# Performance work log

Hardware: AMD Instinct MI355X
Metric: run time of the kernel (lower is better)

The kernel has to match this reference:

```python
import jax, jax.numpy as jnp
import numpy as np

NG = 65160
NM = 10242   # mesh nodes (icosphere splits=5)
N = NG + NM
F = 156      # num_timesteps * num_features = 2 * 78
FI = 3       # init (lat/lon) feature size
H = 128
OUT = 78
B = 2
E_ENC, E_PROC, E_DEC = 130320, 81920, 195480


def gcn_conv(X, src, dst, W, b, num_nodes):
    """PyG GCNConv: add self-loops, symmetric D^-1/2 (A+I) D^-1/2 normalization.
    X: [B, N, Fin]; src/dst: [E] int; W: [Fin, Fout]; b: [Fout]."""
    loop = jnp.arange(num_nodes, dtype=src.dtype)
    s = jnp.concatenate([src, loop])
    d = jnp.concatenate([dst, loop])
    deg = jax.ops.segment_sum(jnp.ones(d.shape, X.dtype), d, num_segments=num_nodes)
    dinv = jax.lax.rsqrt(deg)  # deg >= 1 thanks to self-loops
    norm = dinv[s] * dinv[d]   # [E+N]
    XW = X @ W                 # [B, N, Fout]
    msg = XW[:, s, :] * norm[None, :, None]          # gather + scale
    agg = jax.vmap(lambda m: jax.ops.segment_sum(m, d, num_segments=num_nodes))(msg)
    return agg + b


def mlp2(X, w1, b1, w2, b2):
    return jax.nn.relu(X @ w1 + b1) @ w2 + b2


def setup_inputs() -> dict:
    key = jax.random.key(0)
    ks = jax.random.split(key, 32)
    def w(k, i, o):
        return jax.random.normal(k, (i, o), jnp.float32) / np.float32(np.sqrt(i))
    def bvec(k, o):
        return jax.random.normal(k, (o,), jnp.float32) * 0.01
    inp = {
        'X': jax.random.normal(ks[0], (B, NG, F), jnp.float32),
        'init_grid_features': jax.random.normal(ks[1], (NG, FI), jnp.float32),
        'init_mesh_features': jax.random.normal(ks[2], (NM, FI), jnp.float32),
        'enc_mlp_w1': w(ks[3], F + FI, H), 'enc_mlp_b1': bvec(ks[4], H),
        'enc_mlp_w2': w(ks[5], H, H),      'enc_mlp_b2': bvec(ks[6], H),
        'enc_gcn_w1': w(ks[7], H, H),      'enc_gcn_b1': bvec(ks[8], H),
        'enc_gcn_w2': w(ks[9], H, H),      'enc_gcn_b2': bvec(ks[10], H),
        'proc_gcn_w1': w(ks[11], H, H),    'proc_gcn_b1': bvec(ks[12], H),
        'proc_gcn_w2': w(ks[13], H, H),    'proc_gcn_b2': bvec(ks[14], H),
        'dec_gcn_w1': w(ks[15], H, H),     'dec_gcn_b1': bvec(ks[16], H),
        'dec_gcn_w2': w(ks[17], H, OUT),   'dec_gcn_b2': bvec(ks[18], OUT),
        # encoding graph: bipartite grid -> mesh (mesh indices offset by NG)
        'enc_src': jax.random.randint(ks[19], (E_ENC,), 0, NG, jnp.int32),
        'enc_dst': NG + jax.random.randint(ks[20], (E_ENC,), 0, NM, jnp.int32),
        # processing graph: mesh -> mesh (local indices over mesh nodes)
        'proc_src': jax.random.randint(ks[21], (E_PROC,), 0, NM, jnp.int32),
        'proc_dst': jax.random.randint(ks[22], (E_PROC,), 0, NM, jnp.int32),
        # decoding graph: bipartite mesh -> grid
        'dec_src': NG + jax.random.randint(ks[23], (E_DEC,), 0, NM, jnp.int32),
        'dec_dst': jax.random.randint(ks[24], (E_DEC,), 0, NG, jnp.int32),
    }
    return inp


def reference(X, init_grid_features, init_mesh_features,
              enc_mlp_w1, enc_mlp_b1, enc_mlp_w2, enc_mlp_b2,
              enc_gcn_w1, enc_gcn_b1, enc_gcn_w2, enc_gcn_b2,
              proc_gcn_w1, proc_gcn_b1, proc_gcn_w2, proc_gcn_b2,
              dec_gcn_w1, dec_gcn_b1, dec_gcn_w2, dec_gcn_b2,
              enc_src, enc_dst, proc_src, proc_dst, dec_src, dec_dst):
    b = X.shape[0]
    # _preprocess_input: grid feats + init grid feats ; zero mesh feats + init mesh feats
    grid = jnp.concatenate(
        [X, jnp.broadcast_to(init_grid_features[None], (b, NG, FI))], axis=-1)
    mesh = jnp.concatenate(
        [jnp.zeros((b, NM, F), X.dtype),
         jnp.broadcast_to(init_mesh_features[None], (b, NM, FI))], axis=-1)
    Xall = jnp.concatenate([grid, mesh], axis=1)  # [B, N, F+FI]
    # encoder: MLP then 2-layer GCN on full (grid+mesh) node set
    h = mlp2(Xall, enc_mlp_w1, enc_mlp_b1, enc_mlp_w2, enc_mlp_b2)
    h = jax.nn.relu(gcn_conv(h, enc_src, enc_dst, enc_gcn_w1, enc_gcn_b1, N))
    h = gcn_conv(h, enc_src, enc_dst, enc_gcn_w2, enc_gcn_b2, N)
    grid_h, mesh_h = h[:, :NG, :], h[:, NG:, :]
    # processor: 2-layer GCN on mesh nodes only
    m = jax.nn.relu(gcn_conv(mesh_h, proc_src, proc_dst, proc_gcn_w1, proc_gcn_b1, NM))
    m = gcn_conv(m, proc_src, proc_dst, proc_gcn_w2, proc_gcn_b2, NM)
    # decoder: 2-layer GCN on concatenated (grid, processed mesh) nodes
    pf = jnp.concatenate([grid_h, m], axis=1)  # [B, N, H]
    d1 = jax.nn.relu(gcn_conv(pf, dec_src, dec_dst, dec_gcn_w1, dec_gcn_b1, N))
    out = gcn_conv(d1, dec_src, dec_dst, dec_gcn_w2, dec_gcn_b2, N)
    return out[:, :NG, :]  # [B, NG, OUT]
```

## Files before the change

### kernel.cpp

```cpp
#include <hip/hip_runtime.h>
#include <hip/hip_bf16.h>

#define NGRID  65160
#define NMESH  10242
#define NTOT   75402
#define FEAT   156
#define FI_    3
#define KENC   159
#define HD     128
#define OUTD   78
#define BB     2
#define NE_ENC 130320
#define NE_PROC 81920
#define NE_DEC 195480

typedef __attribute__((ext_vector_type(8))) short bf16x8;
typedef __attribute__((ext_vector_type(4))) float f32x4;

__device__ __forceinline__ short bf16_rtn(float v) {
    unsigned u = __builtin_bit_cast(unsigned, v);
    u += 0x7FFFu + ((u >> 16) & 1u);
    return (short)(u >> 16);
}
__device__ __forceinline__ float bf16_f32(short s) {
    unsigned u = ((unsigned)(unsigned short)s) << 16;
    return __builtin_bit_cast(float, u);
}

__global__ void wprep_kernel(const float* __restrict__ W, int K, int Nc,
                             short* __restrict__ WTh, short* __restrict__ WTl,
                             int KP, int NP)
{
    int idx = blockIdx.x * 256 + threadIdx.x;
    if (idx >= KP * NP) return;
    int c = idx / KP;
    int k = idx - c * KP;
    float v = (k < K && c < Nc) ? W[k * Nc + c] : 0.0f;
    short h = bf16_rtn(v);
    WTh[idx] = h;
    WTl[idx] = bf16_rtn(v - bf16_f32(h));
}

__global__ void zero_kernel(int* __restrict__ p, int n) {
    int i = blockIdx.x * 256 + threadIdx.x;
    if (i < n) p[i] = 0;
}

__global__ void count_kernel(const int* __restrict__ dst, int* __restrict__ cnt, int ne) {
    int e = blockIdx.x * 256 + threadIdx.x;
    if (e < ne) atomicAdd(&cnt[dst[e]], 1);
}

__global__ __launch_bounds__(256)
void scan1_kernel(const int* __restrict__ in, int* __restrict__ out,
                  int* __restrict__ bsum, int n)
{
    __shared__ int ws[256];
    const int t = threadIdx.x;
    const int base = blockIdx.x * 1024 + t * 4;
    int v[4], s = 0;
#pragma unroll
    for (int j = 0; j < 4; ++j) {
        int i = base + j;
        v[j] = (i < n) ? in[i] : 0;
        s += v[j];
    }
    ws[t] = s;
    __syncthreads();
    for (int off = 1; off < 256; off <<= 1) {
        int x = (t >= off) ? ws[t - off] : 0;
        __syncthreads();
        ws[t] += x;
        __syncthreads();
    }
    int excl = ws[t] - s;
#pragma unroll
    for (int j = 0; j < 4; ++j) {
        int i = base + j;
        if (i < n) out[i] = excl;
        excl += v[j];
    }
    if (t == 255) bsum[blockIdx.x] = ws[255];
}

__global__ __launch_bounds__(256)
void scan2_kernel(int* __restrict__ bsum, int nb)
{
    __shared__ int ws[256];
    const int t = threadIdx.x;
    int s = (t < nb) ? bsum[t] : 0;
    ws[t] = s;
    __syncthreads();
    for (int off = 1; off < 256; off <<= 1) {
        int x = (t >= off) ? ws[t - off] : 0;
        __syncthreads();
        ws[t] += x;
        __syncthreads();
    }
    if (t < nb) bsum[t] = ws[t] - s;
}

__global__ __launch_bounds__(256)
void scan3_kernel(int* __restrict__ out, const int* __restrict__ bsum, int n)
{
    int i = blockIdx.x * 256 + threadIdx.x;
    if (i < n) out[i] += bsum[i >> 10];
}

__global__ void dinv_kernel(const int* __restrict__ cnt, float* __restrict__ dinv, int n) {
    int i = blockIdx.x * 256 + threadIdx.x;
    if (i < n) dinv[i] = rsqrtf(1.0f + (float)cnt[i]);
}

__global__ void fillcsr_kernel(const int* __restrict__ src, const int* __restrict__ dst,
                               const int* __restrict__ rowptr, int* __restrict__ fill,
                               int* __restrict__ colsrc, int ne) {
    int e = blockIdx.x * 256 + threadIdx.x;
    if (e < ne) {
        int d = dst[e];
        int pos = atomicAdd(&fill[d], 1);
        colsrc[rowptr[d] + pos] = src[e];
    }
}

template<int KP, int NOUT, int MODE, int RELU_OUT>
__global__ __launch_bounds__(256)
void gemm_mfma(const float* __restrict__ A0, long long a0_bs,
               const float* __restrict__ A1, long long a1_bs, int split,
               const float* __restrict__ Xin, const float* __restrict__ GFin,
               const float* __restrict__ MFin,
               const short* __restrict__ WTh, const short* __restrict__ WTl,
               const float* __restrict__ bias,
               float* __restrict__ Qout, long long q_bs,
               int rows_per_batch, int total_rows)
{
    constexpr int NCT = (NOUT + 15) / 16;
    const int t = threadIdx.x;
    const int w = t >> 6;
    const int l = t & 63;
    const int lane15 = l & 15;
    const int g = l >> 4;

    const int gr_a = blockIdx.x * 64 + w * 16 + lane15;
    const bool a_valid = (gr_a < total_rows);
    int b_a = 0, r_a = 0;
    const float* arow = nullptr;
    if (a_valid) {
        b_a = gr_a / rows_per_batch;
        r_a = gr_a - b_a * rows_per_batch;
        if (MODE == 0) {
            arow = A0 + b_a * a0_bs + (long long)r_a * KP;
        } else if (MODE == 2) {
            if (r_a >= split) arow = A1 + b_a * a1_bs + (long long)(r_a - split) * KP;
            else              arow = A0 + b_a * a0_bs + (long long)r_a * KP;
        }
    }

    f32x4 acc[NCT];
#pragma unroll
    for (int ct = 0; ct < NCT; ++ct) acc[ct] = (f32x4){0.f, 0.f, 0.f, 0.f};

#pragma unroll
    for (int k0 = 0; k0 < KP; k0 += 32) {
        const int kbase = k0 + g * 8;
        float av[8];
        if (MODE == 1) {
#pragma unroll
            for (int j = 0; j < 8; ++j) av[j] = 0.0f;
            if (a_valid) {
                const bool gridr = (r_a < NGRID);
                if (gridr && kbase + 8 <= FEAT) {
                    const float* xrow = Xin + ((long long)b_a * NGRID + r_a) * FEAT + kbase;
#pragma unroll
                    for (int j2 = 0; j2 < 4; ++j2) {
                        float2 v = *(const float2*)(xrow + j2 * 2);
                        av[j2 * 2]     = v.x;
                        av[j2 * 2 + 1] = v.y;
                    }
                } else {
#pragma unroll
                    for (int j = 0; j < 8; ++j) {
                        int k = kbase + j;
                        float v = 0.0f;
                        if (k < FEAT) {
                            if (gridr) v = Xin[((long long)b_a * NGRID + r_a) * FEAT + k];
                        } else if (k < KENC) {
                            v = gridr ? GFin[r_a * FI_ + (k - FEAT)]
                                      : MFin[(r_a - NGRID) * FI_ + (k - FEAT)];
                        }
                        av[j] = v;
                    }
                }
            }
        } else {
            if (a_valid) {
                float4 v0 = *(const float4*)(arow + kbase);
                float4 v1 = *(const float4*)(arow + kbase + 4);
                av[0] = v0.x; av[1] = v0.y; av[2] = v0.z; av[3] = v0.w;
                av[4] = v1.x; av[5] = v1.y; av[6] = v1.z; av[7] = v1.w;
            } else {
#pragma unroll
                for (int j = 0; j < 8; ++j) av[j] = 0.0f;
            }
        }

        bf16x8 ah, al;
#pragma unroll
        for (int j = 0; j < 8; ++j) {
            float v = av[j];
            short h = bf16_rtn(v);
            ah[j] = h;
            al[j] = bf16_rtn(v - bf16_f32(h));
        }

#pragma unroll
        for (int ct = 0; ct < NCT; ++ct) {
            const long long boff = (long long)(ct * 16 + lane15) * KP + kbase;
            bf16x8 bh = *(const bf16x8*)(WTh + boff);
            bf16x8 bl = *(const bf16x8*)(WTl + boff);
            acc[ct] = __builtin_amdgcn_mfma_f32_16x16x32_bf16(ah, bh, acc[ct], 0, 0, 0);
            acc[ct] = __builtin_amdgcn_mfma_f32_16x16x32_bf16(al, bh, acc[ct], 0, 0, 0);
            acc[ct] = __builtin_amdgcn_mfma_f32_16x16x32_bf16(ah, bl, acc[ct], 0, 0, 0);
        }
    }

#pragma unroll
    for (int i = 0; i < 4; ++i) {
        const int gr = blockIdx.x * 64 + w * 16 + g * 4 + i;
        if (gr >= total_rows) continue;
        const int b = gr / rows_per_batch;
        const int r = gr - b * rows_per_batch;
        float* qrow = Qout + b * q_bs + (long long)r * NOUT;
#pragma unroll
        for (int ct = 0; ct < NCT; ++ct) {
            const int c = ct * 16 + lane15;
            if ((NOUT % 16 != 0) && c >= NOUT) continue;
            float v = acc[ct][i];
            if (bias) v += bias[c];
            if (RELU_OUT) v = fmaxf(v, 0.0f);
            qrow[c] = v;
        }
    }
}

template<int NC, int RELU>
__global__ __launch_bounds__(256)
void gather_kernel(const float* __restrict__ Q, long long q_bs,
                   const float* __restrict__ dinv,
                   const int* __restrict__ cnt, const int* __restrict__ rowptr,
                   const int* __restrict__ colsrc,
                   const float* __restrict__ bias,
                   float* __restrict__ Out, long long out_bs, int out_rows)
{
    const int wv = blockIdx.x * 4 + (threadIdx.x >> 6);
    const int lane = threadIdx.x & 63;
    if (wv >= out_rows * BB) return;
    const int b = wv / out_rows;
    const int d = wv - b * out_rows;
    const float dv = dinv[d];
    const float dv2 = dv * dv;
    const int beg = rowptr[d];
    const int num = cnt[d];
    const float* Qb = Q + b * q_bs;

    if (NC == 128) {
        const int c = lane * 2;
        float2 acc = *(const float2*)(Qb + (long long)d * NC + c);
        acc.x *= dv2; acc.y *= dv2;
        for (int e = 0; e < num; ++e) {
            int s = colsrc[beg + e];
            float ns = dinv[s] * dv;
            float2 v = *(const float2*)(Qb + (long long)s * NC + c);
            acc.x += v.x * ns;
            acc.y += v.y * ns;
        }
        acc.x += bias[c]; acc.y += bias[c + 1];
        if (RELU) { acc.x = fmaxf(acc.x, 0.f); acc.y = fmaxf(acc.y, 0.f); }
        *(float2*)(Out + b * out_bs + (long long)d * NC + c) = acc;
    } else {
        const int c1 = lane, c2 = lane + 64;
        const float* qd = Qb + (long long)d * NC;
        float a1 = qd[c1] * dv2;
        float a2 = (c2 < NC) ? qd[c2] * dv2 : 0.f;
        for (int e = 0; e < num; ++e) {
            int s = colsrc[beg + e];
            float ns = dinv[s] * dv;
            const float* qs = Qb + (long long)s * NC;
            a1 += qs[c1] * ns;
            if (c2 < NC) a2 += qs[c2] * ns;
        }
        float* od = Out + b * out_bs + (long long)d * NC;
        a1 += bias[c1];
        if (RELU) a1 = fmaxf(a1, 0.f);
        od[c1] = a1;
        if (c2 < NC) {
            a2 += bias[c2];
            if (RELU) a2 = fmaxf(a2, 0.f);
            od[c2] = a2;
        }
    }
}

static inline int ceil_div(long long a, int b) { return (int)((a + b - 1) / b); }

extern "C" void kernel_launch(void* const* d_in, const int* in_sizes, int n_in,
                              void* d_out, int out_size, void* d_ws, size_t ws_size,
                              hipStream_t stream)
{
    const float* X    = (const float*)d_in[0];
    const float* GF   = (const float*)d_in[1];
    const float* MF   = (const float*)d_in[2];
    const float* emw1 = (const float*)d_in[3];
    const float* emb1 = (const float*)d_in[4];
    const float* emw2 = (const float*)d_in[5];
    const float* emb2 = (const float*)d_in[6];
    const float* egw1 = (const float*)d_in[7];
    const float* egb1 = (const float*)d_in[8];
    const float* egw2 = (const float*)d_in[9];
    const float* egb2 = (const float*)d_in[10];
    const float* pgw1 = (const float*)d_in[11];
    const float* pgb1 = (const float*)d_in[12];
    const float* pgw2 = (const float*)d_in[13];
    const float* pgb2 = (const float*)d_in[14];
    const float* dgw1 = (const float*)d_in[15];
    const float* dgb1 = (const float*)d_in[16];
    const float* dgw2 = (const float*)d_in[17];
    const float* dgb2 = (const float*)d_in[18];
    const int* enc_src = (const int*)d_in[19];
    const int* enc_dst = (const int*)d_in[20];
    const int* proc_src = (const int*)d_in[21];
    const int* proc_dst = (const int*)d_in[22];
    const int* dec_src = (const int*)d_in[23];
    const int* dec_dst = (const int*)d_in[24];
    float* out = (float*)d_out;

    float* ws_f = (float*)d_ws;
    const long long BNH = (long long)BB * NTOT * HD;
    const long long BMH = (long long)BB * NMESH * HD;
    float* Abuf = ws_f;
    float* Bbuf = Abuf + BNH;
    float* mw   = Bbuf + BNH;
    float* m1   = mw + BMH;
    float* dinv_enc  = m1 + BMH;
    float* dinv_proc = dinv_enc + NTOT;
    float* dinv_dec  = dinv_proc + NMESH;
    long long fcnt = 2 * BNH + 2 * BMH + (long long)(NTOT + NMESH + NTOT);
    fcnt = (fcnt + 3) & ~3LL;
    int* ip = (int*)(ws_f + fcnt);
    int* cnt_enc  = ip;
    int* fill_enc = cnt_enc + NTOT;
    int* cnt_proc = fill_enc + NTOT;
    int* fill_proc= cnt_proc + NMESH;
    int* cnt_dec  = fill_proc + NMESH;
    int* fill_dec = cnt_dec + NTOT;
    const long long ZERON = 4LL * NTOT + 2LL * NMESH;
    int* row_enc  = fill_dec + NTOT;
    int* row_proc = row_enc + NTOT;
    int* row_dec  = row_proc + NMESH;
    int* col_enc  = row_dec + NTOT;
    int* col_proc = col_enc + NE_ENC;
    int* col_dec  = col_proc + NE_PROC;
    int* bsum_enc  = col_dec + NE_DEC;
    int* bsum_proc = bsum_enc + 256;
    int* bsum_dec  = bsum_proc + 256;
    long long icnt = ZERON + 2LL * NTOT + NMESH + NE_ENC + NE_PROC + NE_DEC + 768;
    icnt = (icnt + 7) & ~7LL;
    short* wt = (short*)(ip + icnt);

    const int KP1 = 160, NP1 = 128;
    const int KPH = 128, NPH = 128;
    const int NPO = 80;
    short* wt_emw1_h = wt;                      short* wt_emw1_l = wt_emw1_h + NP1 * KP1;
    short* wt_emw2_h = wt_emw1_l + NP1 * KP1;   short* wt_emw2_l = wt_emw2_h + NPH * KPH;
    short* wt_egw1_h = wt_emw2_l + NPH * KPH;   short* wt_egw1_l = wt_egw1_h + NPH * KPH;
    short* wt_egw2_h = wt_egw1_l + NPH * KPH;   short* wt_egw2_l = wt_egw2_h + NPH * KPH;
    short* wt_pgw1_h = wt_egw2_l + NPH * KPH;   short* wt_pgw1_l = wt_pgw1_h + NPH * KPH;
    short* wt_pgw2_h = wt_pgw1_l + NPH * KPH;   short* wt_pgw2_l = wt_pgw2_h + NPH * KPH;
    short* wt_dgw1_h = wt_pgw2_l + NPH * KPH;   short* wt_dgw1_l = wt_dgw1_h + NPH * KPH;
    short* wt_dgw2_h = wt_dgw1_l + NPH * KPH;   short* wt_dgw2_l = wt_dgw2_h + NPO * KPH;

    wprep_kernel<<<ceil_div(NP1 * KP1, 256), 256, 0, stream>>>(emw1, KENC, HD, wt_emw1_h, wt_emw1_l, KP1, NP1);
    wprep_kernel<<<ceil_div(NPH * KPH, 256), 256, 0, stream>>>(emw2, HD, HD, wt_emw2_h, wt_emw2_l, KPH, NPH);
    wprep_kernel<<<ceil_div(NPH * KPH, 256), 256, 0, stream>>>(egw1, HD, HD, wt_egw1_h, wt_egw1_l, KPH, NPH);
    wprep_kernel<<<ceil_div(NPH * KPH, 256), 256, 0, stream>>>(egw2, HD, HD, wt_egw2_h, wt_egw2_l, KPH, NPH);
    wprep_kernel<<<ceil_div(NPH * KPH, 256), 256, 0, stream>>>(pgw1, HD, HD, wt_pgw1_h, wt_pgw1_l, KPH, NPH);
    wprep_kernel<<<ceil_div(NPH * KPH, 256), 256, 0, stream>>>(pgw2, HD, HD, wt_pgw2_h, wt_pgw2_l, KPH, NPH);
    wprep_kernel<<<ceil_div(NPH * KPH, 256), 256, 0, stream>>>(dgw1, HD, HD, wt_dgw1_h, wt_dgw1_l, KPH, NPH);
    wprep_kernel<<<ceil_div(NPO * KPH, 256), 256, 0, stream>>>(dgw2, HD, OUTD, wt_dgw2_h, wt_dgw2_l, KPH, NPO);

    zero_kernel<<<ceil_div(ZERON, 256), 256, 0, stream>>>(cnt_enc, (int)ZERON);
    count_kernel<<<ceil_div(NE_ENC, 256), 256, 0, stream>>>(enc_dst, cnt_enc, NE_ENC);
    count_kernel<<<ceil_div(NE_PROC, 256), 256, 0, stream>>>(proc_dst, cnt_proc, NE_PROC);
    count_kernel<<<ceil_div(NE_DEC, 256), 256, 0, stream>>>(dec_dst, cnt_dec, NE_DEC);
    const int NB_N = ceil_div(NTOT, 1024);
    const int NB_M = ceil_div(NMESH, 1024);
    scan1_kernel<<<NB_N, 256, 0, stream>>>(cnt_enc, row_enc, bsum_enc, NTOT);
    scan1_kernel<<<NB_M, 256, 0, stream>>>(cnt_proc, row_proc, bsum_proc, NMESH);
    scan1_kernel<<<NB_N, 256, 0, stream>>>(cnt_dec, row_dec, bsum_dec, NTOT);
    scan2_kernel<<<1, 256, 0, stream>>>(bsum_enc, NB_N);
    scan2_kernel<<<1, 256, 0, stream>>>(bsum_proc, NB_M);
    scan2_kernel<<<1, 256, 0, stream>>>(bsum_dec, NB_N);
    scan3_kernel<<<ceil_div(NTOT, 256), 256, 0, stream>>>(row_enc, bsum_enc, NTOT);
    scan3_kernel<<<ceil_div(NMESH, 256), 256, 0, stream>>>(row_proc, bsum_proc, NMESH);
    scan3_kernel<<<ceil_div(NTOT, 256), 256, 0, stream>>>(row_dec, bsum_dec, NTOT);
    dinv_kernel<<<ceil_div(NTOT, 256), 256, 0, stream>>>(cnt_enc, dinv_enc, NTOT);
    dinv_kernel<<<ceil_div(NMESH, 256), 256, 0, stream>>>(cnt_proc, dinv_proc, NMESH);
    dinv_kernel<<<ceil_div(NTOT, 256), 256, 0, stream>>>(cnt_dec, dinv_dec, NTOT);
    fillcsr_kernel<<<ceil_div(NE_ENC, 256), 256, 0, stream>>>(enc_src, enc_dst, row_enc, fill_enc, col_enc, NE_ENC);
    fillcsr_kernel<<<ceil_div(NE_PROC, 256), 256, 0, stream>>>(proc_src, proc_dst, row_proc, fill_proc, col_proc, NE_PROC);
    fillcsr_kernel<<<ceil_div(NE_DEC, 256), 256, 0, stream>>>(dec_src, dec_dst, row_dec, fill_dec, col_dec, NE_DEC);

    const int ROWS_N = BB * NTOT;
    const int ROWS_M = BB * NMESH;
    const int GB_N = ceil_div(ROWS_N, 64);
    const int GB_M = ceil_div(ROWS_M, 64);
    const long long NH_BS = (long long)NTOT * HD;
    const long long MH_BS = (long long)NMESH * HD;
    const int GA_N = ceil_div(NTOT * BB, 4);
    const int GA_M = ceil_div(NMESH * BB, 4);
    const int GA_G = ceil_div(NGRID * BB, 4);

    gemm_mfma<160, HD, 1, 1><<<GB_N, 256, 0, stream>>>(
        nullptr, 0, nullptr, 0, 0, X, GF, MF, wt_emw1_h, wt_emw1_l,
        emb1, Abuf, NH_BS, NTOT, ROWS_N);
    gemm_mfma<HD, HD, 0, 0><<<GB_N, 256, 0, stream>>>(
        Abuf, NH_BS, nullptr, 0, 0, nullptr, nullptr, nullptr, wt_emw2_h, wt_emw2_l,
        emb2, Abuf, NH_BS, NTOT, ROWS_N);

    gemm_mfma<HD, HD, 0, 0><<<GB_N, 256, 0, stream>>>(
        Abuf, NH_BS, nullptr, 0, 0, nullptr, nullptr, nullptr, wt_egw1_h, wt_egw1_l,
        nullptr, Bbuf, NH_BS, NTOT, ROWS_N);
    gather_kernel<HD, 1><<<GA_N, 256, 0, stream>>>(
        Bbuf, NH_BS, dinv_enc, cnt_enc, row_enc, col_enc, egb1, Abuf, NH_BS, NTOT);

    gemm_mfma<HD, HD, 0, 0><<<GB_N, 256, 0, stream>>>(
        Abuf, NH_BS, nullptr, 0, 0, nullptr, nullptr, nullptr, wt_egw2_h, wt_egw2_l,
        nullptr, Bbuf, NH_BS, NTOT, ROWS_N);
    gather_kernel<HD, 0><<<GA_N, 256, 0, stream>>>(
        Bbuf, NH_BS, dinv_enc, cnt_enc, row_enc, col_enc, egb2, Abuf, NH_BS, NTOT);

    gemm_mfma<HD, HD, 0, 0><<<GB_M, 256, 0, stream>>>(
        Abuf + (long long)NGRID * HD, NH_BS, nullptr, 0, 0, nullptr, nullptr, nullptr,
        wt_pgw1_h, wt_pgw1_l, nullptr, mw, MH_BS, NMESH, ROWS_M);
    gather_kernel<HD, 1><<<GA_M, 256, 0, stream>>>(
        mw, MH_BS, dinv_proc, cnt_proc, row_proc, col_proc, pgb1, m1, MH_BS, NMESH);

    gemm_mfma<HD, HD, 0, 0><<<GB_M, 256, 0, stream>>>(
        m1, MH_BS, nullptr, 0, 0, nullptr, nullptr, nullptr, wt_pgw2_h, wt_pgw2_l,
        nullptr, mw, MH_BS, NMESH, ROWS_M);
    gather_kernel<HD, 0><<<GA_M, 256, 0, stream>>>(
        mw, MH_BS, dinv_proc, cnt_proc, row_proc, col_proc, pgb2, m1, MH_BS, NMESH);

    gemm_mfma<HD, HD, 2, 0><<<GB_N, 256, 0, stream>>>(
        Abuf, NH_BS, m1, MH_BS, NGRID, nullptr, nullptr, nullptr, wt_dgw1_h, wt_dgw1_l,
        nullptr, Bbuf, NH_BS, NTOT, ROWS_N);
    gather_kernel<HD, 1><<<GA_N, 256, 0, stream>>>(
        Bbuf, NH_BS, dinv_dec, cnt_dec, row_dec, col_dec, dgb1, Abuf, NH_BS, NTOT);

    const long long NO_BS = (long long)NTOT * OUTD;
    const long long GO_BS = (long long)NGRID * OUTD;
    gemm_mfma<HD, OUTD, 0, 0><<<GB_N, 256, 0, stream>>>(
        Abuf, NH_BS, nullptr, 0, 0, nullptr, nullptr, nullptr, wt_dgw2_h, wt_dgw2_l,
        nullptr, Bbuf, NO_BS, NTOT, ROWS_N);
    gather_kernel<OUTD, 0><<<GA_G, 256, 0, stream>>>(
        Bbuf, NO_BS, dinv_dec, cnt_dec, row_dec, col_dec, dgb2, out, GO_BS, NGRID);
}
```

Measured before the change: 1.140 ms.

## Retile MFMA GEMM so each wave computes a 64-row by multi-column-tile block

The GEMM kernel is restructured so each wave covers four 16-row tiles and a subset of column tiles, instead of one 16-row tile across all columns. The hi/lo bf16 weight fragments are loaded once per k-step and reused across the four row tiles, which cuts repeated weight fetches. Blocks now cover 128 rows (256 rows for the 78-column output GEMM). A __syncthreads is added before the stores so the in-place GEMM does not overwrite rows another wave is still reading. The cost is that A rows are now loaded by two waves for the 128-wide outputs, the register footprint grows, and there are fewer blocks.

```diff
diff --git a/kernel.cpp b/kernel.cpp
--- a/kernel.cpp
+++ b/kernel.cpp
@@ -123,7 +123,7 @@
     }
 }
 
-template<int KP, int NOUT, int MODE, int RELU_OUT>
+template<int KP, int NOUTP, int NOUT, int NCW, int MODE, int RELU_OUT>
 __global__ __launch_bounds__(256)
 void gemm_mfma(const float* __restrict__ A0, long long a0_bs,
                const float* __restrict__ A1, long long a1_bs, int split,
@@ -134,111 +134,139 @@
                float* __restrict__ Qout, long long q_bs,
                int rows_per_batch, int total_rows)
 {
-    constexpr int NCT = (NOUT + 15) / 16;
+    constexpr int NCT = NOUTP / 16;
+    constexpr int CW  = NCT / NCW;
+    constexpr int RW  = 4 / CW;
+    constexpr int BROWS = RW * 64;
     const int t = threadIdx.x;
     const int w = t >> 6;
     const int l = t & 63;
     const int lane15 = l & 15;
     const int g = l >> 4;
-
-    const int gr_a = blockIdx.x * 64 + w * 16 + lane15;
-    const bool a_valid = (gr_a < total_rows);
-    int b_a = 0, r_a = 0;
-    const float* arow = nullptr;
-    if (a_valid) {
-        b_a = gr_a / rows_per_batch;
-        r_a = gr_a - b_a * rows_per_batch;
-        if (MODE == 0) {
-            arow = A0 + b_a * a0_bs + (long long)r_a * KP;
-        } else if (MODE == 2) {
-            if (r_a >= split) arow = A1 + b_a * a1_bs + (long long)(r_a - split) * KP;
-            else              arow = A0 + b_a * a0_bs + (long long)r_a * KP;
-        }
-    }
-
-    f32x4 acc[NCT];
-#pragma unroll
-    for (int ct = 0; ct < NCT; ++ct) acc[ct] = (f32x4){0.f, 0.f, 0.f, 0.f};
+    const int rw = w / CW;
+    const int cw = w - rw * CW;
+    const int row_base = blockIdx.x * BROWS + rw * 64;
+    const int ct0 = cw * NCW;
+
+    const float* arow[4];
+    int b_a[4], r_a[4];
+    bool valid[4];
+#pragma unroll
+    for (int m = 0; m < 4; ++m) {
+        const int gr = row_base + m * 16 + lane15;
+        valid[m] = (gr < total_rows);
+        arow[m] = nullptr;
+        b_a[m] = 0; r_a[m] = 0;
+        if (valid[m]) {
+            int b = gr / rows_per_batch;
+            int r = gr - b * rows_per_batch;
+            b_a[m] = b; r_a[m] = r;
+            if (MODE == 0) {
+                arow[m] = A0 + b * a0_bs + (long long)r * KP;
+            } else if (MODE == 2) {
+                if (r >= split) arow[m] = A1 + b * a1_bs + (long long)(r - split) * KP;
+                else            arow[m] = A0 + b * a0_bs + (long long)r * KP;
+            }
+        }
+    }
+
+    f32x4 acc[4][NCW];
+#pragma unroll
+    for (int m = 0; m < 4; ++m)
+#pragma unroll
+        for (int ct = 0; ct < NCW; ++ct) acc[m][ct] = (f32x4){0.f, 0.f, 0.f, 0.f};
 
 #pragma unroll
     for (int k0 = 0; k0 < KP; k0 += 32) {
         const int kbase = k0 + g * 8;
-        float av[8];
-        if (MODE == 1) {
-#pragma unroll
-            for (int j = 0; j < 8; ++j) av[j] = 0.0f;
-            if (a_valid) {
-                const bool gridr = (r_a < NGRID);
-                if (gridr && kbase + 8 <= FEAT) {
-                    const float* xrow = Xin + ((long long)b_a * NGRID + r_a) * FEAT + kbase;
-#pragma unroll
-                    for (int j2 = 0; j2 < 4; ++j2) {
-                        float2 v = *(const float2*)(xrow + j2 * 2);
-                        av[j2 * 2]     = v.x;
-                        av[j2 * 2 + 1] = v.y;
-                    }
-                } else {
-#pragma unroll
-                    for (int j = 0; j < 8; ++j) {
-                        int k = kbase + j;
-                        float v = 0.0f;
-                        if (k < FEAT) {
-                            if (gridr) v = Xin[((long long)b_a * NGRID + r_a) * FEAT + k];
-                        } else if (k < KENC) {
-                            v = gridr ? GFin[r_a * FI_ + (k - FEAT)]
-                                      : MFin[(r_a - NGRID) * FI_ + (k - FEAT)];
+        bf16x8 bh[NCW], bl[NCW];
+#pragma unroll
+        for (int ct = 0; ct < NCW; ++ct) {
+            const long long boff = (long long)((ct0 + ct) * 16 + lane15) * KP + kbase;
+            bh[ct] = *(const bf16x8*)(WTh + boff);
+            bl[ct] = *(const bf16x8*)(WTl + boff);
+        }
+#pragma unroll
+        for (int m = 0; m < 4; ++m) {
+            float av[8];
+            if (MODE == 1) {
+#pragma unroll
+                for (int j = 0; j < 8; ++j) av[j] = 0.0f;
+                if (valid[m]) {
+                    const bool gridr = (r_a[m] < NGRID);
+                    if (gridr && kbase + 8 <= FEAT) {
+                        const float* xrow = Xin + ((long long)b_a[m] * NGRID + r_a[m]) * FEAT + kbase;
+#pragma unroll
+                        for (int j2 = 0; j2 < 4; ++j2) {
+                            float2 v = *(const float2*)(xrow + j2 * 2);
+                            av[j2 * 2]     = v.x;
+                            av[j2 * 2 + 1] = v.y;
                         }
-                        av[j] = v;
+                    } else {
+#pragma unroll
+                        for (int j = 0; j < 8; ++j) {
+                            int k = kbase + j;
+                            float v = 0.0f;
+                            if (k < FEAT) {
+                                if (gridr) v = Xin[((long long)b_a[m] * NGRID + r_a[m]) * FEAT + k];
+                            } else if (k < KENC) {
+                                v = gridr ? GFin[r_a[m] * FI_ + (k - FEAT)]
+                                          : MFin[(r_a[m] - NGRID) * FI_ + (k - FEAT)];
+                            }
+                            av[j] = v;
+                        }
                     }
                 }
+            } else {
+                if (valid[m]) {
+                    float4 v0 = *(const float4*)(arow[m] + kbase);
+                    float4 v1 = *(const float4*)(arow[m] + kbase + 4);
+                    av[0] = v0.x; av[1] = v0.y; av[2] = v0.z; av[3] = v0.w;
+                    av[4] = v1.x; av[5] = v1.y; av[6] = v1.z; av[7] = v1.w;
+                } else {
+#pragma unroll
+                    for (int j = 0; j < 8; ++j) av[j] = 0.0f;
+                }
             }
-        } else {
-            if (a_valid) {
-                float4 v0 = *(const float4*)(arow + kbase);
-                float4 v1 = *(const float4*)(arow + kbase + 4);
-                av[0] = v0.x; av[1] = v0.y; av[2] = v0.z; av[3] = v0.w;
-                av[4] = v1.x; av[5] = v1.y; av[6] = v1.z; av[7] = v1.w;
-            } else {
-#pragma unroll
-                for (int j = 0; j < 8; ++j) av[j] = 0.0f;
+
+            bf16x8 ah, al;
+#pragma unroll
+            for (int j = 0; j < 8; ++j) {
+                float v = av[j];
+                short h = bf16_rtn(v);
+                ah[j] = h;
+                al[j] = bf16_rtn(v - bf16_f32(h));
             }
-        }
-
-        bf16x8 ah, al;
-#pragma unroll
-        for (int j = 0; j < 8; ++j) {
-            float v = av[j];
-            short h = bf16_rtn(v);
-            ah[j] = h;
-            al[j] = bf16_rtn(v - bf16_f32(h));
-        }
-
-#pragma unroll
-        for (int ct = 0; ct < NCT; ++ct) {
-            const long long boff = (long long)(ct * 16 + lane15) * KP + kbase;
-            bf16x8 bh = *(const bf16x8*)(WTh + boff);
-            bf16x8 bl = *(const bf16x8*)(WTl + boff);
-            acc[ct] = __builtin_amdgcn_mfma_f32_16x16x32_bf16(ah, bh, acc[ct], 0, 0, 0);
-            acc[ct] = __builtin_amdgcn_mfma_f32_16x16x32_bf16(al, bh, acc[ct], 0, 0, 0);
-            acc[ct] = __builtin_amdgcn_mfma_f32_16x16x32_bf16(ah, bl, acc[ct], 0, 0, 0);
-        }
-    }
-
-#pragma unroll
-    for (int i = 0; i < 4; ++i) {
-        const int gr = blockIdx.x * 64 + w * 16 + g * 4 + i;
-        if (gr >= total_rows) continue;
-        const int b = gr / rows_per_batch;
-        const int r = gr - b * rows_per_batch;
-        float* qrow = Qout + b * q_bs + (long long)r * NOUT;
-#pragma unroll
-        for (int ct = 0; ct < NCT; ++ct) {
-            const int c = ct * 16 + lane15;
-            if ((NOUT % 16 != 0) && c >= NOUT) continue;
-            float v = acc[ct][i];
-            if (bias) v += bias[c];
-            if (RELU_OUT) v = fmaxf(v, 0.0f);
-            qrow[c] = v;
+
+#pragma unroll
+            for (int ct = 0; ct < NCW; ++ct) {
+                acc[m][ct] = __builtin_amdgcn_mfma_f32_16x16x32_bf16(ah, bh[ct], acc[m][ct], 0, 0, 0);
+                acc[m][ct] = __builtin_amdgcn_mfma_f32_16x16x32_bf16(al, bh[ct], acc[m][ct], 0, 0, 0);
+                acc[m][ct] = __builtin_amdgcn_mfma_f32_16x16x32_bf16(ah, bl[ct], acc[m][ct], 0, 0, 0);
+            }
+        }
+    }
+
+    __syncthreads();
+
+#pragma unroll
+    for (int m = 0; m < 4; ++m) {
+#pragma unroll
+        for (int i = 0; i < 4; ++i) {
+            const int gr = row_base + m * 16 + g * 4 + i;
+            if (gr >= total_rows) continue;
+            const int b = gr / rows_per_batch;
+            const int r = gr - b * rows_per_batch;
+            float* qrow = Qout + b * q_bs + (long long)r * NOUT;
+#pragma unroll
+            for (int ct = 0; ct < NCW; ++ct) {
+                const int c = (ct0 + ct) * 16 + lane15;
+                if ((NOUT != NOUTP) && c >= NOUT) continue;
+                float v = acc[m][ct][i];
+                if (bias) v += bias[c];
+                if (RELU_OUT) v = fmaxf(v, 0.0f);
+                qrow[c] = v;
+            }
         }
     }
 }
@@ -412,46 +440,47 @@
 
     const int ROWS_N = BB * NTOT;
     const int ROWS_M = BB * NMESH;
-    const int GB_N = ceil_div(ROWS_N, 64);
-    const int GB_M = ceil_div(ROWS_M, 64);
+    const int GB_N128 = ceil_div(ROWS_N, 128);
+    const int GB_M128 = ceil_div(ROWS_M, 128);
+    const int GB_N256 = ceil_div(ROWS_N, 256);
     const long long NH_BS = (long long)NTOT * HD;
     const long long MH_BS = (long long)NMESH * HD;
     const int GA_N = ceil_div(NTOT * BB, 4);
     const int GA_M = ceil_div(NMESH * BB, 4);
     const int GA_G = ceil_div(NGRID * BB, 4);
 
-    gemm_mfma<160, HD, 1, 1><<<GB_N, 256, 0, stream>>>(
+    gemm_mfma<160, HD, HD, 4, 1, 1><<<GB_N128, 256, 0, stream>>>(
         nullptr, 0, nullptr, 0, 0, X, GF, MF, wt_emw1_h, wt_emw1_l,
         emb1, Abuf, NH_BS, NTOT, ROWS_N);
-    gemm_mfma<HD, HD, 0, 0><<<GB_N, 256, 0, stream>>>(
+    gemm_mfma<HD, HD, HD, 4, 0, 0><<<GB_N128, 256, 0, stream>>>(
         Abuf, NH_BS, nullptr, 0, 0, nullptr, nullptr, nullptr, wt_emw2_h, wt_emw2_l,
         emb2, Abuf, NH_BS, NTOT, ROWS_N);
 
-    gemm_mfma<HD, HD, 0, 0><<<GB_N, 256, 0, stream>>>(
+    gemm_mfma<HD, HD, HD, 4, 0, 0><<<GB_N128, 256, 0, stream>>>(
         Abuf, NH_BS, nullptr, 0, 0, nullptr, nullptr, nullptr, wt_egw1_h, wt_egw1_l,
         nullptr, Bbuf, NH_BS, NTOT, ROWS_N);
     gather_kernel<HD, 1><<<GA_N, 256, 0, stream>>>(
         Bbuf, NH_BS, dinv_enc, cnt_enc, row_enc, col_enc, egb1, Abuf, NH_BS, NTOT);
 
-    gemm_mfma<HD, HD, 0, 0><<<GB_N, 256, 0, stream>>>(
+    gemm_mfma<HD, HD, HD, 4, 0, 0><<<GB_N128, 256, 0, stream>>>(
         Abuf, NH_BS, nullptr, 0, 0, nullptr, nullptr, nullptr, wt_egw2_h, wt_egw2_l,
         nullptr, Bbuf, NH_BS, NTOT, ROWS_N);
     gather_kernel<HD, 0><<<GA_N, 256, 0, stream>>>(
         Bbuf, NH_BS, dinv_enc, cnt_enc, row_enc, col_enc, egb2, Abuf, NH_BS, NTOT);
 
-    gemm_mfma<HD, HD, 0, 0><<<GB_M, 256, 0, stream>>>(
+    gemm_mfma<HD, HD, HD, 4, 0, 0><<<GB_M128, 256, 0, stream>>>(
         Abuf + (long long)NGRID * HD, NH_BS, nullptr, 0, 0, nullptr, nullptr, nullptr,
         wt_pgw1_h, wt_pgw1_l, nullptr, mw, MH_BS, NMESH, ROWS_M);
     gather_kernel<HD, 1><<<GA_M, 256, 0, stream>>>(
         mw, MH_BS, dinv_proc, cnt_proc, row_proc, col_proc, pgb1, m1, MH_BS, NMESH);
 
-    gemm_mfma<HD, HD, 0, 0><<<GB_M, 256, 0, stream>>>(
+    gemm_mfma<HD, HD, HD, 4, 0, 0><<<GB_M128, 256, 0, stream>>>(
         m1, MH_BS, nullptr, 0, 0, nullptr, nullptr, nullptr, wt_pgw2_h, wt_pgw2_l,
         nullptr, mw, MH_BS, NMESH, ROWS_M);
     gather_kernel<HD, 0><<<GA_M, 256, 0, stream>>>(
         mw, MH_BS, dinv_proc, cnt_proc, row_proc, col_proc, pgb2, m1, MH_BS, NMESH);
 
-    gemm_mfma<HD, HD, 2, 0><<<GB_N, 256, 0, stream>>>(
+    gemm_mfma<HD, HD, HD, 4, 2, 0><<<GB_N128, 256, 0, stream>>>(
         Abuf, NH_BS, m1, MH_BS, NGRID, nullptr, nullptr, nullptr, wt_dgw1_h, wt_dgw1_l,
         nullptr, Bbuf, NH_BS, NTOT, ROWS_N);
     gather_kernel<HD, 1><<<GA_N, 256, 0, stream>>>(
@@ -459,7 +488,7 @@
 
     const long long NO_BS = (long long)NTOT * OUTD;
     const long long GO_BS = (long long)NGRID * OUTD;
-    gemm_mfma<HD, OUTD, 0, 0><<<GB_N, 256, 0, stream>>>(
+    gemm_mfma<HD, 80, OUTD, 5, 0, 0><<<GB_N256, 256, 0, stream>>>(
         Abuf, NH_BS, nullptr, 0, 0, nullptr, nullptr, nullptr, wt_dgw2_h, wt_dgw2_l,
         nullptr, Bbuf, NO_BS, NTOT, ROWS_N);
     gather_kernel<OUTD, 0><<<GA_G, 256, 0, stream>>>(
```

After: 1.124 ms. No clear change (-1.4%).
